# Performance work log

Hardware: AMD Instinct MI355X
Metric: run time of the kernel (lower is better)

## Reference

```python
import jax, jax.numpy as jnp
import numpy as np

B, N, C = 32, 577, 768
H = 12
D = C // H


def setup_inputs() -> dict:
    key = jax.random.key(0)
    ks = jax.random.split(key, 4)
    x = jax.random.normal(ks[0], (B, N, C), dtype=jnp.float32)
    w_qkv = jax.random.normal(ks[1], (C, 3 * C), dtype=jnp.float32) * (C ** -0.5)
    b_qkv = jnp.zeros((3 * C,), dtype=jnp.float32)
    # per-head learnable scale, initialized to head_dim**-0.5 scaled ones
    scale = jnp.ones((H,), dtype=jnp.float32) * (D ** -0.5)
    w_proj = jax.random.normal(ks[2], (C, C), dtype=jnp.float32) * (C ** -0.5)
    b_proj = jnp.zeros((C,), dtype=jnp.float32)
    return {"x": x, "w_qkv": w_qkv, "b_qkv": b_qkv, "scale": scale,
            "w_proj": w_proj, "b_proj": b_proj}


def reference(x, w_qkv, b_qkv, scale, w_proj, b_proj):
    b, n, c = x.shape
    h = scale.shape[0]
    d = c // h
    # fused QKV projection -> [b, n, 3, h, d]
    qkv = (x @ w_qkv + b_qkv).reshape(b, n, 3, h, d)
    q = qkv[:, :, 0]  # [b, n, h, d]
    k = qkv[:, :, 1]
    v = qkv[:, :, 2]
    # attention logits with per-head scale
    attn = jnp.einsum('bihd,bjhd->bhij', q, k) * scale[None, :, None, None]
    # custom mask: block self-attention among patch tokens (rows/cols 1:),
    # CLS token (index 0) unaffected
    if n > 1:
        mask = jnp.zeros((n, n), dtype=bool).at[1:, 1:].set(
            jnp.eye(n - 1, dtype=bool))
        attn = jnp.where(mask[None, None], -jnp.inf, attn)
    attn = jax.nn.softmax(attn, axis=-1)
    out = jnp.einsum('bhij,bjhd->bihd', attn, v).reshape(b, n, c)
    return out @ w_proj + b_proj
```

## Files before the change

kernel.cpp:

```cpp
#include <hip/hip_runtime.h>
#include <math.h>

#define HD 64
#define KVBLK 64
#define LP 72

typedef __attribute__((ext_vector_type(8))) short short8;
typedef __attribute__((ext_vector_type(4))) short short4v;
typedef __attribute__((ext_vector_type(4))) float f32x4;

__device__ __forceinline__ short f2bf(float f) {
    union { float f; unsigned u; } in;
    in.f = f;
    unsigned r = (in.u + 0x7fff + ((in.u >> 16) & 1)) >> 16;
    return (short)r;
}

__global__ __launch_bounds__(256) void convert_bf16(const float* __restrict__ in,
                                                    short* __restrict__ out, long n4) {
    long i = blockIdx.x * 256L + threadIdx.x;
    if (i >= n4) return;
    float4 v = reinterpret_cast<const float4*>(in)[i];
    short4v o;
    o[0] = f2bf(v.x); o[1] = f2bf(v.y); o[2] = f2bf(v.z); o[3] = f2bf(v.w);
    reinterpret_cast<short4v*>(out)[i] = o;
}

__global__ __launch_bounds__(256) void transpose_bf16(const float* __restrict__ in,
                                                      short* __restrict__ out, int K, int N) {
    __shared__ float tile[32][33];
    const int n0 = blockIdx.x * 32, k0 = blockIdx.y * 32;
    const int tx = threadIdx.x & 31, ty = threadIdx.x >> 5;
    #pragma unroll
    for (int i = ty; i < 32; i += 8)
        tile[i][tx] = in[(size_t)(k0 + i) * N + n0 + tx];
    __syncthreads();
    #pragma unroll
    for (int i = ty; i < 32; i += 8)
        out[(size_t)(n0 + i) * K + k0 + tx] = f2bf(tile[tx][i]);
}

template <typename OutT>
__global__ __launch_bounds__(256) void gemm_bf16(const short* __restrict__ A,
                                                 const short* __restrict__ Bt,
                                                 const float* __restrict__ bias,
                                                 OutT* __restrict__ C,
                                                 int M, int N, int K, int nbn) {
    __shared__ short As[2][128 * 64];
    __shared__ short Bs[2][128 * 64];
    const int tid = threadIdx.x;
    const int w = tid >> 6, lane = tid & 63;
    const int g = lane >> 4, l16 = lane & 15;

    const int nwg = gridDim.x;
    const int q = nwg >> 3, r = nwg & 7;
    const int xcd = blockIdx.x & 7, loc = blockIdx.x >> 3;
    const int wgid = (xcd < r ? xcd * (q + 1) : r * (q + 1) + (xcd - r) * q) + loc;
    const int bm = wgid / nbn, bn = wgid % nbn;
    const int m0 = bm * 128, n0 = bn * 128;
    const int wm = (w >> 1) * 64, wn = (w & 1) * 64;

    f32x4 acc[4][4] = {};

    const int lr = lane >> 3;
    const int lc = (lane & 7) * 8;
    const int NT = K >> 6;

    auto stage = [&](int buf, int k0) {
        #pragma unroll
        for (int t = 0; t < 4; ++t) {
            const int rr = 32 * w + 8 * t + lr;
            long arow = m0 + rr; if (arow > M - 1) arow = M - 1;
            const short* ga = A + arow * K + k0 + lc;
            const short* gb = Bt + (size_t)(n0 + rr) * K + k0 + lc;
            __builtin_amdgcn_global_load_lds(
                (const __attribute__((address_space(1))) unsigned*)ga,
                (__attribute__((address_space(3))) unsigned*)&As[buf][(32 * w + 8 * t) * 64],
                16, 0, 0);
            __builtin_amdgcn_global_load_lds(
                (const __attribute__((address_space(1))) unsigned*)gb,
                (__attribute__((address_space(3))) unsigned*)&Bs[buf][(32 * w + 8 * t) * 64],
                16, 0, 0);
        }
    };

    stage(0, 0);
    __syncthreads();

    for (int kt = 0; kt < NT; ++kt) {
        const int cur = kt & 1;
        if (kt + 1 < NT) stage(cur ^ 1, (kt + 1) * 64);

        #pragma unroll
        for (int ks = 0; ks < 2; ++ks) {
            short8 af[4], bfr[4];
            #pragma unroll
            for (int mi = 0; mi < 4; ++mi)
                af[mi] = *reinterpret_cast<const short8*>(
                    &As[cur][(wm + mi * 16 + l16) * 64 + ks * 32 + g * 8]);
            #pragma unroll
            for (int ni = 0; ni < 4; ++ni)
                bfr[ni] = *reinterpret_cast<const short8*>(
                    &Bs[cur][(wn + ni * 16 + l16) * 64 + ks * 32 + g * 8]);
            __builtin_amdgcn_s_setprio(1);
            #pragma unroll
            for (int mi = 0; mi < 4; ++mi)
                #pragma unroll
                for (int ni = 0; ni < 4; ++ni)
                    acc[mi][ni] = __builtin_amdgcn_mfma_f32_16x16x32_bf16(
                        af[mi], bfr[ni], acc[mi][ni], 0, 0, 0);
            __builtin_amdgcn_s_setprio(0);
        }
        __syncthreads();
    }

    float bv[4];
    #pragma unroll
    for (int ni = 0; ni < 4; ++ni) bv[ni] = bias[n0 + wn + ni * 16 + l16];
    #pragma unroll
    for (int mi = 0; mi < 4; ++mi) {
        #pragma unroll
        for (int rr = 0; rr < 4; ++rr) {
            const int row = m0 + wm + mi * 16 + g * 4 + rr;
            if (row < M) {
                #pragma unroll
                for (int ni = 0; ni < 4; ++ni) {
                    float val = acc[mi][ni][rr] + bv[ni];
                    if constexpr (__is_same(OutT, float))
                        C[(size_t)row * N + n0 + wn + ni * 16 + l16] = val;
                    else
                        C[(size_t)row * N + n0 + wn + ni * 16 + l16] = f2bf(val);
                }
            }
        }
    }
}

__global__ __launch_bounds__(256) void flash_attn(const short* __restrict__ qkvb,
                                                  const float* __restrict__ scale,
                                                  short* __restrict__ out) {
    constexpr int Nn = 577, Cc = 768, C3 = 2304, NQB = 10, NH = 12;
    constexpr int NT = 10;
    const int bid = blockIdx.x;
    const int swz = (bid & 7) * 480 + (bid >> 3);
    const int q0 = (swz % NQB) * 64;
    const int h  = (swz / NQB) % NH;
    const int b  = swz / (NQB * NH);

    const int tid  = threadIdx.x;
    const int w    = tid >> 6;
    const int lane = tid & 63;
    const int g    = lane >> 4;
    const int l16  = lane & 15;

    __shared__ alignas(16) short Ks[2][KVBLK * HD];
    __shared__ alignas(16) short Vts[2][HD][LP];
    __shared__ alignas(16) short Ps[4][16][LP];
    __shared__ float facs[4][16];

    const float sl2 = scale[h] * 1.44269504088896f;
    const short* base = qkvb + (size_t)b * Nn * C3;
    const short* kglob = base + Cc + h * HD;
    const short* vglob = base + 2 * Cc + h * HD;

    const int qrow = q0 + w * 16 + l16;
    const int qr = qrow < Nn ? qrow : Nn - 1;
    const short* qp = base + (size_t)qr * C3 + h * HD;
    short8 aq[2];
    aq[0] = *reinterpret_cast<const short8*>(qp + 8 * g);
    aq[1] = *reinterpret_cast<const short8*>(qp + 32 + 8 * g);

    f32x4 oacc[4] = {};
    float mrun = -INFINITY, lrun = 0.f;

    const int tr = tid >> 2;
    const int tc = (tid & 3) * 16;
    const int kst_row = lane >> 3;
    const int kst_dblk = (lane & 7) ^ (lane >> 3);

    auto stageK = [&](int bufi, int kv0) {
        #pragma unroll
        for (int t = 0; t < 2; ++t) {
            const int i = 2 * w + t;
            int kr = kv0 + 8 * i + kst_row;
            if (kr > Nn - 1) kr = Nn - 1;
            const short* src = kglob + (size_t)kr * C3 + kst_dblk * 8;
            __builtin_amdgcn_global_load_lds(
                (const __attribute__((address_space(1))) unsigned*)src,
                (__attribute__((address_space(3))) unsigned*)&Ks[bufi][i * 512],
                16, 0, 0);
        }
    };

    short8 vr0, vr1;
    auto loadV = [&](int kv0) {
        int kr = kv0 + tr; if (kr > Nn - 1) kr = Nn - 1;
        const short* vsrc = vglob + (size_t)kr * C3 + tc;
        vr0 = *reinterpret_cast<const short8*>(vsrc);
        vr1 = *reinterpret_cast<const short8*>(vsrc + 8);
    };
    auto writeV = [&](int bufi) {
        #pragma unroll
        for (int i = 0; i < 8; ++i) {
            Vts[bufi][tc + i][tr]     = vr0[i];
            Vts[bufi][tc + 8 + i][tr] = vr1[i];
        }
    };

    stageK(0, 0);
    loadV(0);
    asm volatile("s_waitcnt vmcnt(0)" ::: "memory");
    writeV(0);
    __syncthreads();

    for (int t = 0; t < NT; ++t) {
        const int cur = t & 1, nxt = cur ^ 1;
        const int kv0 = t * KVBLK;
        const bool more = (t + 1 < NT);
        if (more) { stageK(nxt, kv0 + KVBLK); loadV(kv0 + KVBLK); }

        f32x4 sacc[4] = {};
        __builtin_amdgcn_s_setprio(1);
        #pragma unroll
        for (int f = 0; f < 4; ++f) {
            #pragma unroll
            for (int c = 0; c < 2; ++c) {
                const int slot = (4 * c + g) ^ (l16 & 7);
                short8 ak = *reinterpret_cast<const short8*>(
                    &Ks[cur][(16 * f + l16) * 64 + slot * 8]);
                sacc[f] = __builtin_amdgcn_mfma_f32_16x16x32_bf16(ak, aq[c], sacc[f], 0, 0, 0);
            }
        }
        __builtin_amdgcn_s_setprio(0);

        const int ig = q0 + w * 16 + l16;
        float s2[4][4];
        #pragma unroll
        for (int f = 0; f < 4; ++f)
            #pragma unroll
            for (int r = 0; r < 4; ++r) {
                const int jg = kv0 + 16 * f + 4 * g + r;
                float s = sacc[f][r] * sl2;
                if (jg >= Nn || (jg == ig && ig >= 1)) s = -INFINITY;
                s2[f][r] = s;
            }

        float mx = s2[0][0];
        #pragma unroll
        for (int f = 0; f < 4; ++f)
            #pragma unroll
            for (int r = 0; r < 4; ++r)
                if (f + r) mx = fmaxf(mx, s2[f][r]);
        mx = fmaxf(mx, __shfl_xor(mx, 16, 64));
        mx = fmaxf(mx, __shfl_xor(mx, 32, 64));

        if (__any(mx > mrun + 8.0f)) {
            const float mnew = fmaxf(mrun, mx);
            const float fac = __builtin_amdgcn_exp2f(mrun - mnew);
            mrun = mnew;
            lrun *= fac;
            if (lane < 16) facs[w][lane] = fac;
            asm volatile("s_waitcnt lgkmcnt(0)" ::: "memory");
            #pragma unroll
            for (int r = 0; r < 4; ++r) {
                const float fr = facs[w][4 * g + r];
                #pragma unroll
                for (int df = 0; df < 4; ++df) oacc[df][r] *= fr;
            }
        }

        float sum = 0.f;
        #pragma unroll
        for (int f = 0; f < 4; ++f)
            #pragma unroll
            for (int r = 0; r < 4; ++r) {
                float p = __builtin_amdgcn_exp2f(s2[f][r] - mrun);
                s2[f][r] = p;
                sum += p;
            }
        sum += __shfl_xor(sum, 16, 64);
        sum += __shfl_xor(sum, 32, 64);
        lrun += sum;

        #pragma unroll
        for (int f = 0; f < 4; ++f) {
            unsigned plo, phi;
            asm("v_cvt_pk_bf16_f32 %0, %1, %2" : "=v"(plo) : "v"(s2[f][0]), "v"(s2[f][1]));
            asm("v_cvt_pk_bf16_f32 %0, %1, %2" : "=v"(phi) : "v"(s2[f][2]), "v"(s2[f][3]));
            unsigned* dst = reinterpret_cast<unsigned*>(&Ps[w][l16][16 * f + 4 * g]);
            dst[0] = plo; dst[1] = phi;
        }
        asm volatile("s_waitcnt lgkmcnt(0)" ::: "memory");

        if (more) {
            asm volatile("s_waitcnt vmcnt(0)" ::: "memory");
            writeV(nxt);
        }

        __builtin_amdgcn_s_setprio(1);
        #pragma unroll
        for (int c = 0; c < 2; ++c) {
            short8 pa = *reinterpret_cast<const short8*>(&Ps[w][l16][32 * c + 8 * g]);
            #pragma unroll
            for (int df = 0; df < 4; ++df) {
                short8 bv = *reinterpret_cast<const short8*>(
                    &Vts[cur][16 * df + l16][32 * c + 8 * g]);
                oacc[df] = __builtin_amdgcn_mfma_f32_16x16x32_bf16(pa, bv, oacc[df], 0, 0, 0);
            }
        }
        __builtin_amdgcn_s_setprio(0);
        __syncthreads();
    }

    if (lane < 16) facs[w][lane] = lrun;
    asm volatile("s_waitcnt lgkmcnt(0)" ::: "memory");
    #pragma unroll
    for (int r = 0; r < 4; ++r) {
        const int og = q0 + w * 16 + g * 4 + r;
        if (og < Nn) {
            const float inv = 1.f / facs[w][4 * g + r];
            #pragma unroll
            for (int df = 0; df < 4; ++df)
                out[(size_t)(b * Nn + og) * Cc + h * HD + 16 * df + l16] =
                    f2bf(oacc[df][r] * inv);
        }
    }
}

extern "C" void kernel_launch(void* const* d_in, const int* in_sizes, int n_in,
                              void* d_out, int out_size, void* d_ws, size_t ws_size,
                              hipStream_t stream) {
    const float* x      = (const float*)d_in[0];
    const float* w_qkv  = (const float*)d_in[1];
    const float* b_qkv  = (const float*)d_in[2];
    const float* scale  = (const float*)d_in[3];
    const float* w_proj = (const float*)d_in[4];
    const float* b_proj = (const float*)d_in[5];
    float* out = (float*)d_out;

    const int B = 32, N = 577, C = 768, H = 12;
    const int M  = B * N;
    const int C3 = 3 * C;
    const int MB = (M + 127) / 128;

    short* qkvb   = (short*)d_ws;
    short* attn_o = qkvb + (size_t)M * C3;
    short* xb     = attn_o + (size_t)M * C;
    short* wqkvT  = xb + (size_t)M * C;
    short* wprojT = wqkvT + (size_t)C3 * C;

    dim3 blk(256);
    const long n4 = (long)M * C / 4;
    convert_bf16<<<dim3((n4 + 255) / 256), blk, 0, stream>>>(x, xb, n4);
    transpose_bf16<<<dim3(C3 / 32, C / 32), blk, 0, stream>>>(w_qkv, wqkvT, C, C3);
    transpose_bf16<<<dim3(C / 32, C / 32), blk, 0, stream>>>(w_proj, wprojT, C, C);

    gemm_bf16<short><<<dim3(MB * (C3 / 128)), blk, 0, stream>>>(
        xb, wqkvT, b_qkv, qkvb, M, C3, C, C3 / 128);

    flash_attn<<<dim3(((N + 63) / 64) * H * B), blk, 0, stream>>>(qkvb, scale, attn_o);

    gemm_bf16<float><<<dim3(MB * (C / 128)), blk, 0, stream>>>(
        attn_o, wprojT, b_proj, out, M, C, C, C / 128);
}
```

Baseline: 289.5 us.

## Pre-transpose V into padded buffer and stage it via direct global-to-LDS loads

Adds a separate kernel that writes V per (batch, head) in d-major layout, padded to 640 keys. The attention kernel can then stage V tiles with asynchronous global_load_lds and an XOR swizzle, like K, instead of register loads followed by scattered LDS transposes. It also applies masking only on the diagonal and last tiles, and folds the softmax scale into an fma inside exp2. The cost is an extra kernel launch plus one extra read and write of V through memory.

Result: faster. 277.1 us (-4.3%).

```diff
diff --git a/kernel.cpp b/kernel.cpp
--- a/kernel.cpp
+++ b/kernel.cpp
@@ -38,6 +38,34 @@
     #pragma unroll
     for (int i = ty; i < 32; i += 8)
         out[(size_t)(n0 + i) * K + k0 + tx] = f2bf(tile[tx][i]);
+}
+
+__global__ __launch_bounds__(256) void transpose_v(const short* __restrict__ qkvb,
+                                                   short* __restrict__ vT) {
+    constexpr int Nn = 577, C3 = 2304, NH = 12, NKP = 640;
+    const int bh = blockIdx.x;
+    const int kt = blockIdx.y;
+    const int b = bh / NH, h = bh % NH;
+    const int tid = threadIdx.x;
+    __shared__ short tile[64][33];
+
+    const int tk = tid >> 3;
+    const int key = kt * 32 + tk;
+    const int d0 = (tid & 7) * 8;
+    short8 v = {0, 0, 0, 0, 0, 0, 0, 0};
+    if (key < Nn)
+        v = *reinterpret_cast<const short8*>(
+            qkvb + (size_t)(b * Nn + key) * C3 + 1536 + h * 64 + d0);
+    #pragma unroll
+    for (int i = 0; i < 8; ++i) tile[d0 + i][tk] = v[i];
+    __syncthreads();
+
+    const int d = tid >> 2;
+    const int kb = (tid & 3) * 8;
+    short8 o;
+    #pragma unroll
+    for (int i = 0; i < 8; ++i) o[i] = tile[d][kb + i];
+    *reinterpret_cast<short8*>(vT + (size_t)(bh * 64 + d) * NKP + kt * 32 + kb) = o;
 }
 
 template <typename OutT>
@@ -137,15 +165,16 @@
 }
 
 __global__ __launch_bounds__(256) void flash_attn(const short* __restrict__ qkvb,
+                                                  const short* __restrict__ vT,
                                                   const float* __restrict__ scale,
                                                   short* __restrict__ out) {
-    constexpr int Nn = 577, Cc = 768, C3 = 2304, NQB = 10, NH = 12;
-    constexpr int NT = 10;
+    constexpr int Nn = 577, Cc = 768, C3 = 2304, NQB = 10, NH = 12, NT = 10, NKP = 640;
     const int bid = blockIdx.x;
     const int swz = (bid & 7) * 480 + (bid >> 3);
     const int q0 = (swz % NQB) * 64;
     const int h  = (swz / NQB) % NH;
     const int b  = swz / (NQB * NH);
+    const int qblk = q0 >> 6;
 
     const int tid  = threadIdx.x;
     const int w    = tid >> 6;
@@ -154,14 +183,15 @@
     const int l16  = lane & 15;
 
     __shared__ alignas(16) short Ks[2][KVBLK * HD];
-    __shared__ alignas(16) short Vts[2][HD][LP];
+    __shared__ alignas(16) short Vts[2][HD * KVBLK];
     __shared__ alignas(16) short Ps[4][16][LP];
     __shared__ float facs[4][16];
 
     const float sl2 = scale[h] * 1.44269504088896f;
+    const float thr = 8.0f / sl2;
     const short* base = qkvb + (size_t)b * Nn * C3;
     const short* kglob = base + Cc + h * HD;
-    const short* vglob = base + 2 * Cc + h * HD;
+    const short* vtb = vT + (size_t)(b * NH + h) * HD * NKP;
 
     const int qrow = q0 + w * 16 + l16;
     const int qr = qrow < Nn ? qrow : Nn - 1;
@@ -171,10 +201,8 @@
     aq[1] = *reinterpret_cast<const short8*>(qp + 32 + 8 * g);
 
     f32x4 oacc[4] = {};
-    float mrun = -INFINITY, lrun = 0.f;
-
-    const int tr = tid >> 2;
-    const int tc = (tid & 3) * 16;
+    float mrun = -INFINITY, m2 = -INFINITY, lrun = 0.f;
+
     const int kst_row = lane >> 3;
     const int kst_dblk = (lane & 7) ^ (lane >> 3);
 
@@ -191,33 +219,29 @@
                 16, 0, 0);
         }
     };
-
-    short8 vr0, vr1;
-    auto loadV = [&](int kv0) {
-        int kr = kv0 + tr; if (kr > Nn - 1) kr = Nn - 1;
-        const short* vsrc = vglob + (size_t)kr * C3 + tc;
-        vr0 = *reinterpret_cast<const short8*>(vsrc);
-        vr1 = *reinterpret_cast<const short8*>(vsrc + 8);
+    auto stageV = [&](int bufi, int kv0) {
+        #pragma unroll
+        for (int t = 0; t < 2; ++t) {
+            const int i = 2 * w + t;
+            const int r = 8 * i + kst_row;
+            const int kb = (lane & 7) ^ (r & 7);
+            const short* src = vtb + (size_t)r * NKP + kv0 + kb * 8;
+            __builtin_amdgcn_global_load_lds(
+                (const __attribute__((address_space(1))) unsigned*)src,
+                (__attribute__((address_space(3))) unsigned*)&Vts[bufi][i * 512],
+                16, 0, 0);
+        }
     };
-    auto writeV = [&](int bufi) {
-        #pragma unroll
-        for (int i = 0; i < 8; ++i) {
-            Vts[bufi][tc + i][tr]     = vr0[i];
-            Vts[bufi][tc + 8 + i][tr] = vr1[i];
-        }
-    };
 
     stageK(0, 0);
-    loadV(0);
-    asm volatile("s_waitcnt vmcnt(0)" ::: "memory");
-    writeV(0);
+    stageV(0, 0);
     __syncthreads();
 
     for (int t = 0; t < NT; ++t) {
         const int cur = t & 1, nxt = cur ^ 1;
         const int kv0 = t * KVBLK;
         const bool more = (t + 1 < NT);
-        if (more) { stageK(nxt, kv0 + KVBLK); loadV(kv0 + KVBLK); }
+        if (more) { stageK(nxt, kv0 + KVBLK); stageV(nxt, kv0 + KVBLK); }
 
         f32x4 sacc[4] = {};
         __builtin_amdgcn_s_setprio(1);
@@ -238,12 +262,17 @@
         #pragma unroll
         for (int f = 0; f < 4; ++f)
             #pragma unroll
-            for (int r = 0; r < 4; ++r) {
-                const int jg = kv0 + 16 * f + 4 * g + r;
-                float s = sacc[f][r] * sl2;
-                if (jg >= Nn || (jg == ig && ig >= 1)) s = -INFINITY;
-                s2[f][r] = s;
-            }
+            for (int r = 0; r < 4; ++r)
+                s2[f][r] = sacc[f][r];
+        if (t == qblk || t == NT - 1) {
+            #pragma unroll
+            for (int f = 0; f < 4; ++f)
+                #pragma unroll
+                for (int r = 0; r < 4; ++r) {
+                    const int jg = kv0 + 16 * f + 4 * g + r;
+                    if (jg >= Nn || (jg == ig && ig >= 1)) s2[f][r] = -INFINITY;
+                }
+        }
 
         float mx = s2[0][0];
         #pragma unroll
@@ -254,10 +283,11 @@
         mx = fmaxf(mx, __shfl_xor(mx, 16, 64));
         mx = fmaxf(mx, __shfl_xor(mx, 32, 64));
 
-        if (__any(mx > mrun + 8.0f)) {
+        if (__any(mx > mrun + thr)) {
             const float mnew = fmaxf(mrun, mx);
-            const float fac = __builtin_amdgcn_exp2f(mrun - mnew);
-            mrun = mnew;
+            const float m2new = mnew * sl2;
+            const float fac = __builtin_amdgcn_exp2f(m2 - m2new);
+            mrun = mnew; m2 = m2new;
             lrun *= fac;
             if (lane < 16) facs[w][lane] = fac;
             asm volatile("s_waitcnt lgkmcnt(0)" ::: "memory");
@@ -274,7 +304,7 @@
         for (int f = 0; f < 4; ++f)
             #pragma unroll
             for (int r = 0; r < 4; ++r) {
-                float p = __builtin_amdgcn_exp2f(s2[f][r] - mrun);
+                float p = __builtin_amdgcn_exp2f(fmaf(s2[f][r], sl2, -m2));
                 s2[f][r] = p;
                 sum += p;
             }
@@ -292,19 +322,15 @@
         }
         asm volatile("s_waitcnt lgkmcnt(0)" ::: "memory");
 
-        if (more) {
-            asm volatile("s_waitcnt vmcnt(0)" ::: "memory");
-            writeV(nxt);
-        }
-
         __builtin_amdgcn_s_setprio(1);
         #pragma unroll
         for (int c = 0; c < 2; ++c) {
             short8 pa = *reinterpret_cast<const short8*>(&Ps[w][l16][32 * c + 8 * g]);
             #pragma unroll
             for (int df = 0; df < 4; ++df) {
+                const int slot = (4 * c + g) ^ (l16 & 7);
                 short8 bv = *reinterpret_cast<const short8*>(
-                    &Vts[cur][16 * df + l16][32 * c + 8 * g]);
+                    &Vts[cur][(16 * df + l16) * 64 + slot * 8]);
                 oacc[df] = __builtin_amdgcn_mfma_f32_16x16x32_bf16(pa, bv, oacc[df], 0, 0, 0);
             }
         }
@@ -348,6 +374,7 @@
     short* xb     = attn_o + (size_t)M * C;
     short* wqkvT  = xb + (size_t)M * C;
     short* wprojT = wqkvT + (size_t)C3 * C;
+    short* vT     = wprojT + (size_t)C * C;
 
     dim3 blk(256);
     const long n4 = (long)M * C / 4;
@@ -358,7 +385,9 @@
     gemm_bf16<short><<<dim3(MB * (C3 / 128)), blk, 0, stream>>>(
         xb, wqkvT, b_qkv, qkvb, M, C3, C, C3 / 128);
 
-    flash_attn<<<dim3(((N + 63) / 64) * H * B), blk, 0, stream>>>(qkvb, scale, attn_o);
+    transpose_v<<<dim3(B * H, 20), blk, 0, stream>>>(qkvb, vT);
+
+    flash_attn<<<dim3(((N + 63) / 64) * H * B), blk, 0, stream>>>(qkvb, vT, scale, attn_o);
 
     gemm_bf16<float><<<dim3(MB * (C / 128)), blk, 0, stream>>>(
         attn_o, wprojT, b_proj, out, M, C, C, C / 128);
```
